# Kernel optimization log

Measured on AMD Instinct MI355X. Metric: run time of the kernel, lower is better.

Reference implementation:

```python
import jax, jax.numpy as jnp
import numpy as np

SCALE = 128.0          # GriddingDistance scale
GRID_MIN = -64.0       # floor(min coord) for points in (-64, 64)
R = 128                # voxels per axis = ceil(max) - floor(min)
G = R * R * R          # flattened grid size per sample

# 8 trilinear corner offsets (8, 3)
_CORNERS = jnp.array([[i, j, k] for i in (0, 1) for j in (0, 1) for k in (0, 1)], dtype=jnp.int32)


def _gridding(cloud):
    """Trilinear scatter of (b, n, 3) scaled points into (b, G) voxel grid.

    Mirrors gridding.forward: per point, weight each of the 8 surrounding
    voxel corners by prod(1 - |p - corner|) and scatter-add into the grid.
    """
    b, n, _ = cloud.shape
    p = cloud - GRID_MIN                     # shift to [0, R)
    x0f = jnp.floor(p)
    d = p - x0f                              # (b, n, 3) fractional offsets
    x0 = x0f.astype(jnp.int32)
    idx = jnp.clip(x0[:, :, None, :] + _CORNERS, 0, R - 1)      # (b, n, 8, 3)
    # corner weight: d for the +1 corner, (1 - d) for the base corner
    w = jnp.where(_CORNERS[None, None] == 1, d[:, :, None, :], 1.0 - d[:, :, None, :])
    w = w.prod(axis=-1)                      # (b, n, 8)
    flat = (idx[..., 0] * R + idx[..., 1]) * R + idx[..., 2]    # (b, n, 8)
    flat = flat + jnp.arange(b, dtype=jnp.int32)[:, None, None] * G
    grid = jnp.zeros(b * G, dtype=cloud.dtype).at[flat.reshape(-1)].add(w.reshape(-1))
    return grid.reshape(b, G)


def setup_inputs() -> dict:
    key = jax.random.key(0)
    k1, k2 = jax.random.split(key)
    # normalized clouds in (-0.49, 0.49) so scaled points stay inside the grid
    pred = (jax.random.uniform(k1, (8, 65536, 3), dtype=jnp.float32) - 0.5) * 0.98
    gt = (jax.random.uniform(k2, (8, 65536, 3), dtype=jnp.float32) - 0.5) * 0.98
    return {"pred_cloud": pred, "gt_cloud": gt}


def reference(pred_cloud, gt_cloud):
    pred_grid = _gridding(pred_cloud * SCALE)
    gt_grid = _gridding(gt_cloud * SCALE)
    return pred_grid, gt_grid
```

## Files before the change

kernel.cpp:

```cpp
#include <hip/hip_runtime.h>


#define RES   128
#define GRIDG (RES * RES * RES)
#define NSLAB 16
#define NREG  256
#define NBIN  (NSLAB * NREG)
#define CAPB  640
#define STAGE_CAP 2048
#define PTS_PER_BLOCK 1024

typedef float floatx4 __attribute__((ext_vector_type(4)));

__device__ __forceinline__ int clampi(int v) {
    return v < 0 ? 0 : (v > RES - 1 ? RES - 1 : v);
}


__global__ __launch_bounds__(256) void place_kernel(
    const float* __restrict__ pred, const float* __restrict__ gt,
    unsigned* __restrict__ cursor,
    float4* __restrict__ bins,
    int npts, int nblkPerSlab)
{
    __shared__ unsigned cnt[NREG];
    __shared__ unsigned scan[NREG];
    __shared__ unsigned curs[NREG];
    __shared__ unsigned gbase[NREG];
    __shared__ __align__(16) float4 stage[STAGE_CAP];

    const int gblk = blockIdx.x;
    const int slab = gblk / nblkPerSlab;
    const int blk  = gblk - slab * nblkPerSlab;
    const float* cloud = (slab < 8) ? pred : gt;
    const float* cbase = cloud + (size_t)(slab & 7) * npts * 3
                               + (size_t)blk * PTS_PER_BLOCK * 3;

    const int t = threadIdx.x;
    cnt[t] = 0;
    __syncthreads();

    float px[4], py[4], pz[4];
    bool valid[4];
    const bool fullBlock = ((blk + 1) * PTS_PER_BLOCK) <= npts;

    if (fullBlock) {
        const float4* b4 = (const float4*)cbase;
        const float4 f0 = b4[3 * t + 0];
        const float4 f1 = b4[3 * t + 1];
        const float4 f2 = b4[3 * t + 2];
        px[0] = f0.x; py[0] = f0.y; pz[0] = f0.z;
        px[1] = f0.w; py[1] = f1.x; pz[1] = f1.y;
        px[2] = f1.z; py[2] = f1.w; pz[2] = f2.x;
        px[3] = f2.y; py[3] = f2.z; pz[3] = f2.w;
#pragma unroll
        for (int k = 0; k < 4; ++k) {
            valid[k] = true;
            px[k] = fmaf(px[k], 128.0f, 64.0f);
            py[k] = fmaf(py[k], 128.0f, 64.0f);
            pz[k] = fmaf(pz[k], 128.0f, 64.0f);
        }
    } else {
#pragma unroll
        for (int k = 0; k < 4; ++k) {
            const int jj = 4 * t + k;
            valid[k] = (blk * PTS_PER_BLOCK + jj < npts);
            if (valid[k]) {
                px[k] = fmaf(cbase[(size_t)jj * 3 + 0], 128.0f, 64.0f);
                py[k] = fmaf(cbase[(size_t)jj * 3 + 1], 128.0f, 64.0f);
                pz[k] = fmaf(cbase[(size_t)jj * 3 + 2], 128.0f, 64.0f);
            } else {
                px[k] = py[k] = pz[k] = 0.0f;
            }
        }
    }

#pragma unroll
    for (int k = 0; k < 4; ++k) {
        if (!valid[k]) continue;
        const int ix = (int)floorf(px[k]), iy = (int)floorf(py[k]);
        const int rx0 = clampi(ix) >> 3, rx1 = clampi(ix + 1) >> 3;
        const int ry0 = clampi(iy) >> 3, ry1 = clampi(iy + 1) >> 3;
        for (int a = rx0; a <= rx1; ++a)
            for (int b = ry0; b <= ry1; ++b)
                atomicAdd(&cnt[(a << 4) | b], 1u);
    }
    __syncthreads();

    unsigned v = cnt[t];
    scan[t] = v;
    __syncthreads();
    for (int d = 1; d < NREG; d <<= 1) {
        unsigned add = (t >= d) ? scan[t - d] : 0u;
        __syncthreads();
        scan[t] += add;
        __syncthreads();
    }

    {
        const unsigned c = cnt[t];
        unsigned base = 0;
        if (c) base = atomicAdd(&cursor[slab * NREG + t], c);
        gbase[t] = base;
        curs[t] = scan[t] - c;
    }
    __syncthreads();

#pragma unroll
    for (int k = 0; k < 4; ++k) {
        if (!valid[k]) continue;
        const float x = px[k], y = py[k], z = pz[k];
        const int ix = (int)floorf(x), iy = (int)floorf(y);
        const int rx0 = clampi(ix) >> 3, rx1 = clampi(ix + 1) >> 3;
        const int ry0 = clampi(iy) >> 3, ry1 = clampi(iy + 1) >> 3;
        for (int a = rx0; a <= rx1; ++a)
            for (int b = ry0; b <= ry1; ++b) {
                const int r = (a << 4) | b;
                const unsigned idx = atomicAdd(&curs[r], 1u);
                if (idx < STAGE_CAP) {
                    float4 e; e.x = x; e.y = y; e.z = z;
                    e.w = __int_as_float(r);
                    stage[idx] = e;
                }
            }
    }
    __syncthreads();

    unsigned total = scan[NREG - 1];
    if (total > STAGE_CAP) total = STAGE_CAP;
    const size_t slabBase = (size_t)slab * NREG * CAPB;
    for (unsigned e = t; e < total; e += 256) {
        float4 f = stage[e];
        const int r = __float_as_int(f.w);
        const unsigned local = e - (scan[r] - cnt[r]);
        const unsigned gslot = gbase[r] + local;
        if (gslot < CAPB) {
            f.w = 0.0f;
            bins[slabBase + (size_t)r * CAPB + gslot] = f;
        }
    }
}


__global__ __launch_bounds__(256) void accum_kernel(
    const float4* __restrict__ bins, const unsigned* __restrict__ cursor,
    float* __restrict__ out)
{
    __shared__ __align__(16) float vox[8 * 8 * 128];

    const int bin  = blockIdx.x;
    const int slab = bin >> 8;
    const int reg  = bin & 255;
    const int rx = reg >> 4, ry = reg & 15;
    const int t = threadIdx.x;

    unsigned n = cursor[bin];
    if (n > CAPB) n = CAPB;

    float4* v4 = (float4*)vox;
    for (int i = t; i < 2048; i += 256) v4[i] = make_float4(0, 0, 0, 0);
    __syncthreads();

    const float4* seg = bins + (size_t)bin * CAPB;
    for (unsigned i = t; i < n; i += 256) {
        const float4 e = seg[i];
        const float x = e.x, y = e.y, z = e.z;
        const float xf = floorf(x), yf = floorf(y), zf = floorf(z);
        const float dx = x - xf, dy = y - yf, dz = z - zf;
        const int ix = (int)xf, iy = (int)yf, iz = (int)zf;
        const int x0 = clampi(ix), x1 = clampi(ix + 1);
        const int y0 = clampi(iy), y1 = clampi(iy + 1);
        const int z0 = clampi(iz), z1 = clampi(iz + 1);
        const float wx0 = 1.0f - dx, wy0 = 1.0f - dy, wz0 = 1.0f - dz;

#pragma unroll
        for (int sx = 0; sx < 2; ++sx) {
            const int cx = sx ? x1 : x0;
            if ((cx >> 3) != rx) continue;
            const float wx = sx ? dx : wx0;
#pragma unroll
            for (int sy = 0; sy < 2; ++sy) {
                const int cy = sy ? y1 : y0;
                if ((cy >> 3) != ry) continue;
                const float wxy = wx * (sy ? dy : wy0);
                const int base = ((cx & 7) << 10) | ((cy & 7) << 7);
                atomicAdd(&vox[base + z0], wxy * wz0);
                atomicAdd(&vox[base + z1], wxy * dz);
            }
        }
    }
    __syncthreads();

    float* gp = out + (size_t)slab * GRIDG
              + ((size_t)rx << 17) + ((size_t)ry << 10);
    const floatx4* lv = (const floatx4*)vox;
    for (int i = t; i < 2048; i += 256) {
        const int l   = i << 2;
        const int lx  = l >> 10;
        const int rem = l & 1023;
        __builtin_nontemporal_store(lv[i],
            (floatx4*)(gp + ((size_t)lx << 14) + rem));
    }
}


__global__ __launch_bounds__(256) void gridding_scatter_kernel(
    const float* __restrict__ cloud, float* __restrict__ grid, int n)
{
    const int j = blockIdx.x * blockDim.x + threadIdx.x;
    if (j >= n) return;
    const int b = blockIdx.y;
    const size_t pt = (size_t)b * n + j;

    const float x = fmaf(cloud[pt * 3 + 0], 128.0f, 64.0f);
    const float y = fmaf(cloud[pt * 3 + 1], 128.0f, 64.0f);
    const float z = fmaf(cloud[pt * 3 + 2], 128.0f, 64.0f);
    const float xf = floorf(x), yf = floorf(y), zf = floorf(z);
    const float dx = x - xf, dy = y - yf, dz = z - zf;
    const int ix = (int)xf, iy = (int)yf, iz = (int)zf;
    const int x0 = clampi(ix), x1 = clampi(ix + 1);
    const int y0 = clampi(iy), y1 = clampi(iy + 1);
    const int z0 = clampi(iz), z1 = clampi(iz + 1);
    const float wx0 = 1.0f - dx, wy0 = 1.0f - dy, wz0 = 1.0f - dz;

    float* gp = grid + (size_t)b * GRIDG;
    const int bx0 = x0 << 14, bx1 = x1 << 14;
    const int by0 = y0 << 7,  by1 = y1 << 7;
    atomicAdd(gp + (bx0 + by0 + z0), wx0 * wy0 * wz0);
    atomicAdd(gp + (bx0 + by0 + z1), wx0 * wy0 * dz);
    atomicAdd(gp + (bx0 + by1 + z0), wx0 * dy * wz0);
    atomicAdd(gp + (bx0 + by1 + z1), wx0 * dy * dz);
    atomicAdd(gp + (bx1 + by0 + z0), dx * wy0 * wz0);
    atomicAdd(gp + (bx1 + by0 + z1), dx * wy0 * dz);
    atomicAdd(gp + (bx1 + by1 + z0), dx * dy * wz0);
    atomicAdd(gp + (bx1 + by1 + z1), dx * dy * dz);
}


extern "C" void kernel_launch(void* const* d_in, const int* in_sizes, int n_in,
                              void* d_out, int out_size, void* d_ws, size_t ws_size,
                              hipStream_t stream) {
    const float* pred = (const float*)d_in[0];
    const float* gt   = (const float*)d_in[1];
    float* out = (float*)d_out;

    const int bsz  = 8;
    const int npts = in_sizes[0] / (bsz * 3);

    const size_t cursorBytes = (size_t)NBIN * sizeof(unsigned);
    const size_t binsBytes   = (size_t)NBIN * CAPB * sizeof(float4);
    const size_t needWs      = cursorBytes + binsBytes;

    if (ws_size >= needWs) {
        unsigned* cursor = (unsigned*)d_ws;
        float4* bins = (float4*)((char*)d_ws + cursorBytes);

        (void)hipMemsetAsync(cursor, 0, cursorBytes, stream);

        const int nblkPerSlab = (npts + PTS_PER_BLOCK - 1) / PTS_PER_BLOCK;
        place_kernel<<<dim3(NSLAB * nblkPerSlab), dim3(256), 0, stream>>>(
            pred, gt, cursor, bins, npts, nblkPerSlab);
        accum_kernel<<<dim3(NBIN), dim3(256), 0, stream>>>(bins, cursor, out);
    } else {
        (void)hipMemsetAsync(d_out, 0, (size_t)out_size * sizeof(float), stream);
        dim3 block(256);
        dim3 grid((npts + 255) / 256, bsz);
        float* pred_grid = out;
        float* gt_grid   = out + (size_t)bsz * GRIDG;
        gridding_scatter_kernel<<<grid, block, 0, stream>>>(pred, pred_grid, npts);
        gridding_scatter_kernel<<<grid, block, 0, stream>>>(gt,   gt_grid,   npts);
    }
}
```

Baseline: 196.1 us.

## Pack binned points as xyz triplets and widen accumulation blocks to 512 threads

The intermediate bin storage drops from padded float4 records to packed 3-float records, and the shared staging buffer in the placement kernel is split into structure-of-arrays with a byte region tag. The aim is to cut global write and read traffic for the bins by a quarter and shrink shared memory use. The accumulation kernel is launched with 512 threads to hide more latency per bin. In exchange, the scalar strided 3-float accesses are less vectorized than float4 loads and stores, and larger blocks may lower occupancy per CU.

```diff
diff --git a/kernel.cpp b/kernel.cpp
--- a/kernel.cpp
+++ b/kernel.cpp
@@ -20,14 +20,17 @@
 __global__ __launch_bounds__(256) void place_kernel(
     const float* __restrict__ pred, const float* __restrict__ gt,
     unsigned* __restrict__ cursor,
-    float4* __restrict__ bins,
+    float* __restrict__ bins,
     int npts, int nblkPerSlab)
 {
     __shared__ unsigned cnt[NREG];
     __shared__ unsigned scan[NREG];
     __shared__ unsigned curs[NREG];
     __shared__ unsigned gbase[NREG];
-    __shared__ __align__(16) float4 stage[STAGE_CAP];
+    __shared__ float sx[STAGE_CAP];
+    __shared__ float sy[STAGE_CAP];
+    __shared__ float sz[STAGE_CAP];
+    __shared__ unsigned char stag[STAGE_CAP];
 
     const int gblk = blockIdx.x;
     const int slab = gblk / nblkPerSlab;
@@ -87,8 +90,7 @@
     }
     __syncthreads();
 
-    unsigned v = cnt[t];
-    scan[t] = v;
+    scan[t] = cnt[t];
     __syncthreads();
     for (int d = 1; d < NREG; d <<= 1) {
         unsigned add = (t >= d) ? scan[t - d] : 0u;
@@ -118,9 +120,8 @@
                 const int r = (a << 4) | b;
                 const unsigned idx = atomicAdd(&curs[r], 1u);
                 if (idx < STAGE_CAP) {
-                    float4 e; e.x = x; e.y = y; e.z = z;
-                    e.w = __int_as_float(r);
-                    stage[idx] = e;
+                    sx[idx] = x; sy[idx] = y; sz[idx] = z;
+                    stag[idx] = (unsigned char)r;
                 }
             }
     }
@@ -130,20 +131,21 @@
     if (total > STAGE_CAP) total = STAGE_CAP;
     const size_t slabBase = (size_t)slab * NREG * CAPB;
     for (unsigned e = t; e < total; e += 256) {
-        float4 f = stage[e];
-        const int r = __float_as_int(f.w);
+        const int r = stag[e];
         const unsigned local = e - (scan[r] - cnt[r]);
         const unsigned gslot = gbase[r] + local;
         if (gslot < CAPB) {
-            f.w = 0.0f;
-            bins[slabBase + (size_t)r * CAPB + gslot] = f;
-        }
-    }
-}
-
-
-__global__ __launch_bounds__(256) void accum_kernel(
-    const float4* __restrict__ bins, const unsigned* __restrict__ cursor,
+            const size_t fo = (slabBase + (size_t)r * CAPB + gslot) * 3;
+            bins[fo + 0] = sx[e];
+            bins[fo + 1] = sy[e];
+            bins[fo + 2] = sz[e];
+        }
+    }
+}
+
+
+__global__ __launch_bounds__(512) void accum_kernel(
+    const float* __restrict__ bins, const unsigned* __restrict__ cursor,
     float* __restrict__ out)
 {
     __shared__ __align__(16) float vox[8 * 8 * 128];
@@ -158,13 +160,14 @@
     if (n > CAPB) n = CAPB;
 
     float4* v4 = (float4*)vox;
-    for (int i = t; i < 2048; i += 256) v4[i] = make_float4(0, 0, 0, 0);
-    __syncthreads();
-
-    const float4* seg = bins + (size_t)bin * CAPB;
-    for (unsigned i = t; i < n; i += 256) {
-        const float4 e = seg[i];
-        const float x = e.x, y = e.y, z = e.z;
+    for (int i = t; i < 2048; i += 512) v4[i] = make_float4(0, 0, 0, 0);
+    __syncthreads();
+
+    const float* seg = bins + (size_t)bin * CAPB * 3;
+    for (unsigned i = t; i < n; i += 512) {
+        const float x = seg[(size_t)i * 3 + 0];
+        const float y = seg[(size_t)i * 3 + 1];
+        const float z = seg[(size_t)i * 3 + 2];
         const float xf = floorf(x), yf = floorf(y), zf = floorf(z);
         const float dx = x - xf, dy = y - yf, dz = z - zf;
         const int ix = (int)xf, iy = (int)yf, iz = (int)zf;
@@ -174,15 +177,15 @@
         const float wx0 = 1.0f - dx, wy0 = 1.0f - dy, wz0 = 1.0f - dz;
 
 #pragma unroll
-        for (int sx = 0; sx < 2; ++sx) {
-            const int cx = sx ? x1 : x0;
+        for (int sxk = 0; sxk < 2; ++sxk) {
+            const int cx = sxk ? x1 : x0;
             if ((cx >> 3) != rx) continue;
-            const float wx = sx ? dx : wx0;
-#pragma unroll
-            for (int sy = 0; sy < 2; ++sy) {
-                const int cy = sy ? y1 : y0;
+            const float wx = sxk ? dx : wx0;
+#pragma unroll
+            for (int syk = 0; syk < 2; ++syk) {
+                const int cy = syk ? y1 : y0;
                 if ((cy >> 3) != ry) continue;
-                const float wxy = wx * (sy ? dy : wy0);
+                const float wxy = wx * (syk ? dy : wy0);
                 const int base = ((cx & 7) << 10) | ((cy & 7) << 7);
                 atomicAdd(&vox[base + z0], wxy * wz0);
                 atomicAdd(&vox[base + z1], wxy * dz);
@@ -194,7 +197,7 @@
     float* gp = out + (size_t)slab * GRIDG
               + ((size_t)rx << 17) + ((size_t)ry << 10);
     const floatx4* lv = (const floatx4*)vox;
-    for (int i = t; i < 2048; i += 256) {
+    for (int i = t; i < 2048; i += 512) {
         const int l   = i << 2;
         const int lx  = l >> 10;
         const int rem = l & 1023;
@@ -248,19 +251,19 @@
     const int npts = in_sizes[0] / (bsz * 3);
 
     const size_t cursorBytes = (size_t)NBIN * sizeof(unsigned);
-    const size_t binsBytes   = (size_t)NBIN * CAPB * sizeof(float4);
+    const size_t binsBytes   = (size_t)NBIN * CAPB * 3 * sizeof(float);
     const size_t needWs      = cursorBytes + binsBytes;
 
     if (ws_size >= needWs) {
         unsigned* cursor = (unsigned*)d_ws;
-        float4* bins = (float4*)((char*)d_ws + cursorBytes);
+        float* bins = (float*)((char*)d_ws + cursorBytes);
 
         (void)hipMemsetAsync(cursor, 0, cursorBytes, stream);
 
         const int nblkPerSlab = (npts + PTS_PER_BLOCK - 1) / PTS_PER_BLOCK;
         place_kernel<<<dim3(NSLAB * nblkPerSlab), dim3(256), 0, stream>>>(
             pred, gt, cursor, bins, npts, nblkPerSlab);
-        accum_kernel<<<dim3(NBIN), dim3(256), 0, stream>>>(bins, cursor, out);
+        accum_kernel<<<dim3(NBIN), dim3(512), 0, stream>>>(bins, cursor, out);
     } else {
         (void)hipMemsetAsync(d_out, 0, (size_t)out_size * sizeof(float), stream);
         dim3 block(256);
```

After: 195.1 us. Within noise of the previous version (-0.5%).
